# Performance work log

Hardware: AMD Instinct MI355X
Metric: run time of the kernel (lower is better)

## Reference

```python
import jax, jax.numpy as jnp
import numpy as np

N_NODES = 100000
N_EDGES = 3200000
NODE_F = 256
EDGE_F = 16
N_HEAD = 8
OUT_F = 256
NEG_SLOPE = 0.2
BN_EPS = 1e-5


def _seg_softmax(e, idx, num_segments):
    # numerically stable segment softmax over edges grouped by idx
    m = jax.ops.segment_max(e, idx, num_segments=num_segments)
    ex = jnp.exp(e - m[idx])
    s = jax.ops.segment_sum(ex, idx, num_segments=num_segments)
    return ex / s[idx]


def setup_inputs() -> dict:
    key = jax.random.key(0)
    ks = jax.random.split(key, 16)
    inp = {}
    inp["feat_src"] = jax.random.normal(ks[0], (N_NODES, NODE_F), jnp.float32)
    inp["feat_edge"] = jax.random.normal(ks[1], (N_EDGES, EDGE_F), jnp.float32)
    inp["src"] = jax.random.randint(ks[2], (N_EDGES,), 0, N_NODES, jnp.int32)
    inp["dst"] = jax.random.randint(ks[3], (N_EDGES,), 0, N_NODES, jnp.int32)
    def xav(k, fan_in, fan_out):
        # xavier_normal with relu gain sqrt(2)
        std = np.sqrt(2.0) * np.sqrt(2.0 / (fan_in + fan_out))
        return jax.random.normal(k, (fan_in, fan_out), jnp.float32) * std
    inp["W_prop_src"] = xav(ks[4], NODE_F, N_HEAD)
    inp["W_attn_src"] = xav(ks[5], NODE_F, N_HEAD)
    inp["W_attn_dst"] = xav(ks[6], NODE_F, N_HEAD)
    inp["W_attn_edge"] = xav(ks[7], EDGE_F, N_HEAD)
    inp["bn_gamma"] = jnp.ones((N_HEAD,), jnp.float32)
    inp["bn_beta"] = jnp.zeros((N_HEAD,), jnp.float32)
    inp["W_agg"] = xav(ks[8], N_HEAD, OUT_F)
    inp["b_agg"] = jnp.zeros((OUT_F,), jnp.float32)
    inp["W_apply_dst"] = xav(ks[9], NODE_F, OUT_F)
    inp["b_apply_dst"] = jnp.zeros((OUT_F,), jnp.float32)
    inp["W_apply"] = xav(ks[10], OUT_F, OUT_F)
    inp["b_apply"] = jnp.zeros((OUT_F,), jnp.float32)
    return inp


def reference(feat_src, feat_edge, src, dst, W_prop_src, W_attn_src, W_attn_dst,
              W_attn_edge, bn_gamma, bn_beta, W_agg, b_agg, W_apply_dst,
              b_apply_dst, W_apply, b_apply):
    leaky = lambda x: jnp.where(x >= 0, x, NEG_SLOPE * x)
    feat_dst = feat_src  # non-block graph
    feat_src_fc = feat_src @ W_prop_src            # [N, H]
    attn_src = feat_src @ W_attn_src               # [N, H]
    attn_dst = feat_dst @ W_attn_dst               # [N, H]
    attn_edge = feat_edge @ W_attn_edge            # [E, H]
    e = attn_src[src] + attn_dst[dst] + attn_edge  # [E, H]
    e = leaky(e)                                   # edge_att_actv = leaky_relu
    # dual softmax: geometric mean of dst- and src-normalized softmaxes
    a_dst = jnp.clip(_seg_softmax(e, dst, N_NODES), 1e-9)
    a_src = jnp.clip(_seg_softmax(e, src, N_NODES), 1e-9)
    a = jnp.sqrt(a_dst * a_src)                    # [E, H]
    msg_sum = jax.ops.segment_sum(feat_src_fc[src] * a, dst, num_segments=N_NODES)  # [N, H]
    # BatchNorm1d (training mode: batch statistics over nodes, biased var)
    mu = jnp.mean(msg_sum, axis=0)
    var = jnp.mean((msg_sum - mu) ** 2, axis=0)
    h = (msg_sum - mu) / jnp.sqrt(var + BN_EPS) * bn_gamma + bn_beta
    rst = h @ W_agg + b_agg                        # [N, OUT]
    rst = rst + feat_dst @ W_apply_dst + b_apply_dst
    rst = leaky(rst)
    rst = rst @ W_apply + b_apply
    return rst
```

## Files before the change

### kernel.cpp

```cpp
#include <hip/hip_runtime.h>

#define LRELU(x) ((x) >= 0.0f ? (x) : 0.2f * (x))

typedef __attribute__((ext_vector_type(8))) short short8;
typedef __attribute__((ext_vector_type(4))) float f32x4;

__device__ __forceinline__ unsigned short f2bf(float f) {
    union { float f; unsigned int u; } v; v.f = f;
    unsigned int u = v.u;
    u += 0x7FFFu + ((u >> 16) & 1u);
    return (unsigned short)(u >> 16);
}

__device__ __forceinline__ float bf2f(unsigned short u) {
    union { unsigned int u; float f; } v; v.u = ((unsigned int)u) << 16;
    return v.f;
}

__global__ __launch_bounds__(256) void k_nodeprep(
    const float* __restrict__ feat,
    const float* __restrict__ Wp, const float* __restrict__ Was,
    const float* __restrict__ Wad,
    float* __restrict__ fc, float* __restrict__ as_t, float* __restrict__ ad_t,
    int N, int gridN8,
    const float* __restrict__ W1, const float* __restrict__ Wagg,
    const float* __restrict__ W2,
    const float* __restrict__ b_agg, const float* __restrict__ b1,
    const float* __restrict__ b2,
    unsigned short* __restrict__ B1t, unsigned short* __restrict__ B2t,
    float* __restrict__ bias1, float* __restrict__ bias2)
{
    if ((int)blockIdx.x >= gridN8) {
        int idx = (blockIdx.x - gridN8) * 256 + threadIdx.x;
        if (idx < 73728) {
            int c = idx >> 13, rem = idx & 8191;
            int n = rem >> 5, k = rem & 31;
            float v;
            if (c < 8) v = W1[(c * 32 + k) * 256 + n];
            else       v = (k < 8) ? Wagg[k * 256 + n] : 0.f;
            B1t[idx] = f2bf(v);
        } else if (idx < 139264) {
            int j = idx - 73728;
            int c = j >> 13, rem = j & 8191;
            int n = rem >> 5, k = rem & 31;
            B2t[j] = f2bf(W2[(c * 32 + k) * 256 + n]);
        } else if (idx < 139520) {
            int n = idx - 139264;
            bias1[n] = b_agg[n] + b1[n];
        } else if (idx < 139776) {
            int n = idx - 139520;
            bias2[n] = b2[n];
        }
        return;
    }
    __shared__ float Wl[3 * 2048];
    for (int i = threadIdx.x; i < 3 * 2048; i += 256) {
        float v;
        if (i < 2048)      v = Wp[i];
        else if (i < 4096) v = Was[i - 2048];
        else               v = Wad[i - 4096];
        Wl[i] = v;
    }
    __syncthreads();
    int gid = blockIdx.x * 256 + threadIdx.x;
    int n = gid >> 3, h = gid & 7;
    if (n >= N) return;
    const float4* f4 = (const float4*)(feat + (size_t)n * 256);
    float aP = 0.f, aS = 0.f, aD = 0.f;
#pragma unroll 8
    for (int k4 = 0; k4 < 64; ++k4) {
        float4 f = f4[k4];
        int b = k4 * 32 + h;
        aP += f.x * Wl[b]        + f.y * Wl[b + 8]        + f.z * Wl[b + 16]        + f.w * Wl[b + 24];
        aS += f.x * Wl[2048 + b] + f.y * Wl[2048 + b + 8] + f.z * Wl[2048 + b + 16] + f.w * Wl[2048 + b + 24];
        aD += f.x * Wl[4096 + b] + f.y * Wl[4096 + b + 8] + f.z * Wl[4096 + b + 16] + f.w * Wl[4096 + b + 24];
    }
    fc[gid] = aP; as_t[gid] = aS; ad_t[gid] = aD;
}

__device__ __forceinline__ float edge_ex(
    const float* __restrict__ feat_edge, const float* Wl,
    const float* __restrict__ as_t, const float* __restrict__ ad_t,
    int e, int h, int s, int d)
{
    const float4* fe = (const float4*)(feat_edge + (size_t)e * 16);
    float4 f0 = fe[0], f1 = fe[1], f2 = fe[2], f3 = fe[3];
    float ae = f0.x * Wl[h]      + f0.y * Wl[h + 8]   + f0.z * Wl[h + 16]  + f0.w * Wl[h + 24]
             + f1.x * Wl[h + 32] + f1.y * Wl[h + 40]  + f1.z * Wl[h + 48]  + f1.w * Wl[h + 56]
             + f2.x * Wl[h + 64] + f2.y * Wl[h + 72]  + f2.z * Wl[h + 80]  + f2.w * Wl[h + 88]
             + f3.x * Wl[h + 96] + f3.y * Wl[h + 104] + f3.z * Wl[h + 112] + f3.w * Wl[h + 120];
    float ev = as_t[(size_t)s * 8 + h] + ad_t[(size_t)d * 8 + h] + ae;
    ev = LRELU(ev);
    return __expf(ev);
}

__global__ __launch_bounds__(256) void k_edge1(
    const float* __restrict__ feat_edge,
    const int* __restrict__ src, const int* __restrict__ dst,
    const float* __restrict__ We,
    const float* __restrict__ as_t, const float* __restrict__ ad_t,
    float* __restrict__ sum_dst, float* __restrict__ sum_src,
    unsigned short* __restrict__ exd, int E)
{
    __shared__ float Wl[128];
    if (threadIdx.x < 128) Wl[threadIdx.x] = We[threadIdx.x];
    __syncthreads();
    int gid = blockIdx.x * 256 + threadIdx.x;
    int e = gid >> 3, h = gid & 7;
    if (e >= E) return;
    int s = src[e], d = dst[e];
    float ex = edge_ex(feat_edge, Wl, as_t, ad_t, e, h, s, d);
    exd[gid] = f2bf(ex);
    atomicAdd(&sum_dst[(size_t)d * 8 + h], ex);
    atomicAdd(&sum_src[(size_t)s * 8 + h], ex);
}

__global__ __launch_bounds__(256) void k_edge2(
    const unsigned short* __restrict__ exd,
    const int* __restrict__ src, const int* __restrict__ dst,
    const float* __restrict__ sum_dst, const float* __restrict__ sum_src,
    const float* __restrict__ fc, float* __restrict__ msg, int E)
{
    int gid = blockIdx.x * 256 + threadIdx.x;
    int e = gid >> 3, h = gid & 7;
    if (e >= E) return;
    int s = src[e], d = dst[e];
    float ex = bf2f(exd[gid]);
    float Sd = sum_dst[(size_t)d * 8 + h];
    float Ss = sum_src[(size_t)s * 8 + h];
    float a_d = fmaxf(ex / Sd, 1e-9f);
    float a_s = fmaxf(ex / Ss, 1e-9f);
    atomicAdd(&msg[(size_t)d * 8 + h], fc[(size_t)s * 8 + h] * sqrtf(a_d * a_s));
}

__global__ __launch_bounds__(256) void k_bn_stats(
    const float* __restrict__ msg, float* __restrict__ accum, int N)
{
    __shared__ float s1[8], s2[8];
    if (threadIdx.x < 8) { s1[threadIdx.x] = 0.f; s2[threadIdx.x] = 0.f; }
    __syncthreads();
    int h = threadIdx.x & 7;
    float a1 = 0.f, a2 = 0.f;
    int total = N * 8;
    for (int i = blockIdx.x * 256 + threadIdx.x; i < total; i += gridDim.x * 256) {
        float x = msg[i];
        a1 += x; a2 += x * x;
    }
    atomicAdd(&s1[h], a1);
    atomicAdd(&s2[h], a2);
    __syncthreads();
    if (threadIdx.x < 8) {
        atomicAdd(&accum[threadIdx.x], s1[threadIdx.x]);
        atomicAdd(&accum[8 + threadIdx.x], s2[threadIdx.x]);
    }
}

#define ASTRIDE 296

__global__ __launch_bounds__(256, 2) void k_fused_apply(
    const float* __restrict__ feat, const float* __restrict__ msg,
    const float* __restrict__ accum,
    const float* __restrict__ gamma, const float* __restrict__ beta,
    const unsigned short* __restrict__ B1t,
    const unsigned short* __restrict__ B2t,
    const float* __restrict__ bias1, const float* __restrict__ bias2,
    float* __restrict__ out, int N)
{
    __shared__ __align__(16) unsigned short As[64 * ASTRIDE];
    __shared__ __align__(16) unsigned short Bs[8192];

    int tid = threadIdx.x;
    int row0 = blockIdx.x * 64;

#pragma unroll
    for (int t = 0; t < 16; ++t) {
        int i = tid + t * 256;
        int r = i >> 6, k4 = i & 63;
        float4 f = make_float4(0.f, 0.f, 0.f, 0.f);
        if (row0 + r < N)
            f = ((const float4*)(feat + (size_t)(row0 + r) * 256))[k4];
        ushort4 b;
        b.x = f2bf(f.x); b.y = f2bf(f.y); b.z = f2bf(f.z); b.w = f2bf(f.w);
        *(ushort4*)&As[r * ASTRIDE + k4 * 4] = b;
    }
#pragma unroll
    for (int t = 0; t < 8; ++t) {
        int e = tid + t * 256;
        int r = e >> 5, c = e & 31;
        float v = 0.f;
        if (c < 8 && row0 + r < N) {
            float invN = 1.0f / (float)N;
            float mu = accum[c] * invN;
            float var = accum[8 + c] * invN - mu * mu;
            float rstd = rsqrtf(var + 1e-5f);
            v = (msg[(size_t)(row0 + r) * 8 + c] - mu) * rstd * gamma[c] + beta[c];
        }
        As[r * ASTRIDE + 256 + c] = f2bf(v);
    }

    int wave = tid >> 6;
    int lane = tid & 63;
    int n16  = lane & 15;
    int quad = lane >> 4;
    int col0 = wave * 64;

    f32x4 acc[4][4];
#pragma unroll
    for (int rt = 0; rt < 4; ++rt)
#pragma unroll
        for (int ct = 0; ct < 4; ++ct)
            acc[rt][ct] = (f32x4){0.f, 0.f, 0.f, 0.f};

    for (int kc = 0; kc < 9; ++kc) {
        __syncthreads();
#pragma unroll
        for (int t = 0; t < 4; ++t) {
            int i = tid + t * 256;
            ((float4*)Bs)[i] = ((const float4*)(B1t + kc * 8192))[i];
        }
        __syncthreads();
        int kbase = kc * 32;
        short8 af[4], bf[4];
#pragma unroll
        for (int rt = 0; rt < 4; ++rt)
            af[rt] = *(const short8*)&As[(rt * 16 + n16) * ASTRIDE + kbase + quad * 8];
#pragma unroll
        for (int ct = 0; ct < 4; ++ct)
            bf[ct] = *(const short8*)&Bs[(col0 + ct * 16 + n16) * 32 + quad * 8];
#pragma unroll
        for (int rt = 0; rt < 4; ++rt)
#pragma unroll
            for (int ct = 0; ct < 4; ++ct)
                acc[rt][ct] = __builtin_amdgcn_mfma_f32_16x16x32_bf16(
                    af[rt], bf[ct], acc[rt][ct], 0, 0, 0);
    }

    float bi[4];
#pragma unroll
    for (int ct = 0; ct < 4; ++ct) bi[ct] = bias1[col0 + ct * 16 + n16];
    __syncthreads();
#pragma unroll
    for (int rt = 0; rt < 4; ++rt)
#pragma unroll
        for (int ct = 0; ct < 4; ++ct)
#pragma unroll
            for (int r = 0; r < 4; ++r) {
                float v = acc[rt][ct][r] + bi[ct];
                v = LRELU(v);
                int row = rt * 16 + quad * 4 + r;
                int col = col0 + ct * 16 + n16;
                As[row * ASTRIDE + col] = f2bf(v);
            }

#pragma unroll
    for (int rt = 0; rt < 4; ++rt)
#pragma unroll
        for (int ct = 0; ct < 4; ++ct)
            acc[rt][ct] = (f32x4){0.f, 0.f, 0.f, 0.f};

    for (int kc = 0; kc < 8; ++kc) {
        __syncthreads();
#pragma unroll
        for (int t = 0; t < 4; ++t) {
            int i = tid + t * 256;
            ((float4*)Bs)[i] = ((const float4*)(B2t + kc * 8192))[i];
        }
        __syncthreads();
        int kbase = kc * 32;
        short8 af[4], bf[4];
#pragma unroll
        for (int rt = 0; rt < 4; ++rt)
            af[rt] = *(const short8*)&As[(rt * 16 + n16) * ASTRIDE + kbase + quad * 8];
#pragma unroll
        for (int ct = 0; ct < 4; ++ct)
            bf[ct] = *(const short8*)&Bs[(col0 + ct * 16 + n16) * 32 + quad * 8];
#pragma unroll
        for (int rt = 0; rt < 4; ++rt)
#pragma unroll
            for (int ct = 0; ct < 4; ++ct)
                acc[rt][ct] = __builtin_amdgcn_mfma_f32_16x16x32_bf16(
                    af[rt], bf[ct], acc[rt][ct], 0, 0, 0);
    }

    float bi2[4];
#pragma unroll
    for (int ct = 0; ct < 4; ++ct) bi2[ct] = bias2[col0 + ct * 16 + n16];
#pragma unroll
    for (int rt = 0; rt < 4; ++rt)
#pragma unroll
        for (int r = 0; r < 4; ++r) {
            int row = row0 + rt * 16 + quad * 4 + r;
            if (row < N) {
#pragma unroll
                for (int ct = 0; ct < 4; ++ct) {
                    int col = col0 + ct * 16 + n16;
                    out[(size_t)row * 256 + col] = acc[rt][ct][r] + bi2[ct];
                }
            }
        }
}

extern "C" void kernel_launch(void* const* d_in, const int* in_sizes, int n_in,
                              void* d_out, int out_size, void* d_ws, size_t ws_size,
                              hipStream_t stream)
{
    const float* feat      = (const float*)d_in[0];
    const float* feat_edge = (const float*)d_in[1];
    const int*   src       = (const int*)d_in[2];
    const int*   dst       = (const int*)d_in[3];
    const float* W_prop    = (const float*)d_in[4];
    const float* W_as      = (const float*)d_in[5];
    const float* W_ad      = (const float*)d_in[6];
    const float* W_edge    = (const float*)d_in[7];
    const float* bn_gamma  = (const float*)d_in[8];
    const float* bn_beta   = (const float*)d_in[9];
    const float* W_agg     = (const float*)d_in[10];
    const float* b_agg     = (const float*)d_in[11];
    const float* W1        = (const float*)d_in[12];
    const float* b1        = (const float*)d_in[13];
    const float* W2        = (const float*)d_in[14];
    const float* b2        = (const float*)d_in[15];
    float* out = (float*)d_out;

    int N = in_sizes[0] / 256;
    int E = in_sizes[2];
    int N8 = N * 8;

    char* base = (char*)d_ws;
    size_t o = 0;
    auto take = [&](size_t bytes) -> char* {
        char* p = base + o;
        o = (o + bytes + 63) & ~(size_t)63;
        return p;
    };
    float* sum_dst = (float*)take((size_t)N8 * sizeof(float));
    float* sum_src = (float*)take((size_t)N8 * sizeof(float));
    float* msg     = (float*)take((size_t)N8 * sizeof(float));
    float* accum   = (float*)take(16 * sizeof(float));
    size_t zero_bytes = o;
    float* fc    = (float*)take((size_t)N8 * sizeof(float));
    float* as_t  = (float*)take((size_t)N8 * sizeof(float));
    float* ad_t  = (float*)take((size_t)N8 * sizeof(float));
    float* bias1 = (float*)take(256 * sizeof(float));
    float* bias2 = (float*)take(256 * sizeof(float));
    unsigned short* B1t = (unsigned short*)take(73728 * sizeof(unsigned short));
    unsigned short* B2t = (unsigned short*)take(65536 * sizeof(unsigned short));
    unsigned short* exd = (unsigned short*)take((size_t)E * 8 * sizeof(unsigned short));
    (void)ws_size;

    hipMemsetAsync(d_ws, 0, zero_bytes, stream);

    int gridN8 = (N8 + 255) / 256;
    int gridE8 = (E * 8 + 255) / 256;
    int gridF  = (N + 63) / 64;

    k_nodeprep<<<gridN8 + 546, 256, 0, stream>>>(
        feat, W_prop, W_as, W_ad, fc, as_t, ad_t, N, gridN8,
        W1, W_agg, W2, b_agg, b1, b2, B1t, B2t, bias1, bias2);
    k_edge1<<<gridE8, 256, 0, stream>>>(feat_edge, src, dst, W_edge,
                                        as_t, ad_t, sum_dst, sum_src, exd, E);
    k_edge2<<<gridE8, 256, 0, stream>>>(exd, src, dst, sum_dst, sum_src,
                                        fc, msg, E);
    k_bn_stats<<<512, 256, 0, stream>>>(msg, accum, N);
    k_fused_apply<<<gridF, 256, 0, stream>>>(feat, msg, accum, bn_gamma, bn_beta,
                                             B1t, B2t, bias1, bias2, out, N);
}
```

Before: 970.3 us.

## Factor dual-softmax normalization out of edge loop into per-node scalings

Rewrites sqrt(ex/Sd * ex/Ss) as ex * rsqrt(Ss) * rsqrt(Sd), so the per-src factor is folded into a precomputed node table g = fc*rsqrt(sum_src) and the per-dst factor is applied once per node in the BN stats pass. The edge kernel then does one gather instead of three (no sum_dst, sum_src or fc gathers per edge) and no divides or sqrt. This drops the 1e-9 clamp on each edge's attention, which changes results only when attention values are tiny. It also adds a small node-level kernel.

```diff
diff --git a/kernel.cpp b/kernel.cpp
--- a/kernel.cpp
+++ b/kernel.cpp
@@ -115,26 +115,31 @@
     atomicAdd(&sum_src[(size_t)s * 8 + h], ex);
 }
 
+__global__ __launch_bounds__(256) void k_gtab(
+    const float* __restrict__ fc, const float* __restrict__ sum_src,
+    float* __restrict__ g, int total)
+{
+    int i = blockIdx.x * 256 + threadIdx.x;
+    if (i >= total) return;
+    g[i] = fc[i] * rsqrtf(fmaxf(sum_src[i], 1e-30f));
+}
+
 __global__ __launch_bounds__(256) void k_edge2(
     const unsigned short* __restrict__ exd,
     const int* __restrict__ src, const int* __restrict__ dst,
-    const float* __restrict__ sum_dst, const float* __restrict__ sum_src,
-    const float* __restrict__ fc, float* __restrict__ msg, int E)
+    const float* __restrict__ g, float* __restrict__ U, int E)
 {
     int gid = blockIdx.x * 256 + threadIdx.x;
     int e = gid >> 3, h = gid & 7;
     if (e >= E) return;
     int s = src[e], d = dst[e];
     float ex = bf2f(exd[gid]);
-    float Sd = sum_dst[(size_t)d * 8 + h];
-    float Ss = sum_src[(size_t)s * 8 + h];
-    float a_d = fmaxf(ex / Sd, 1e-9f);
-    float a_s = fmaxf(ex / Ss, 1e-9f);
-    atomicAdd(&msg[(size_t)d * 8 + h], fc[(size_t)s * 8 + h] * sqrtf(a_d * a_s));
-}
-
-__global__ __launch_bounds__(256) void k_bn_stats(
-    const float* __restrict__ msg, float* __restrict__ accum, int N)
+    atomicAdd(&U[(size_t)d * 8 + h], ex * g[(size_t)s * 8 + h]);
+}
+
+__global__ __launch_bounds__(256) void k_bn_msg(
+    float* __restrict__ msg, const float* __restrict__ sum_dst,
+    float* __restrict__ accum, int N)
 {
     __shared__ float s1[8], s2[8];
     if (threadIdx.x < 8) { s1[threadIdx.x] = 0.f; s2[threadIdx.x] = 0.f; }
@@ -143,8 +148,9 @@
     float a1 = 0.f, a2 = 0.f;
     int total = N * 8;
     for (int i = blockIdx.x * 256 + threadIdx.x; i < total; i += gridDim.x * 256) {
-        float x = msg[i];
-        a1 += x; a2 += x * x;
+        float m = msg[i] * rsqrtf(fmaxf(sum_dst[i], 1e-30f));
+        msg[i] = m;
+        a1 += m; a2 += m * m;
     }
     atomicAdd(&s1[h], a1);
     atomicAdd(&s2[h], a2);
@@ -341,6 +347,7 @@
     float* fc    = (float*)take((size_t)N8 * sizeof(float));
     float* as_t  = (float*)take((size_t)N8 * sizeof(float));
     float* ad_t  = (float*)take((size_t)N8 * sizeof(float));
+    float* g     = (float*)take((size_t)N8 * sizeof(float));
     float* bias1 = (float*)take(256 * sizeof(float));
     float* bias2 = (float*)take(256 * sizeof(float));
     unsigned short* B1t = (unsigned short*)take(73728 * sizeof(unsigned short));
@@ -359,9 +366,9 @@
         W1, W_agg, W2, b_agg, b1, b2, B1t, B2t, bias1, bias2);
     k_edge1<<<gridE8, 256, 0, stream>>>(feat_edge, src, dst, W_edge,
                                         as_t, ad_t, sum_dst, sum_src, exd, E);
-    k_edge2<<<gridE8, 256, 0, stream>>>(exd, src, dst, sum_dst, sum_src,
-                                        fc, msg, E);
-    k_bn_stats<<<512, 256, 0, stream>>>(msg, accum, N);
+    k_gtab<<<gridN8, 256, 0, stream>>>(fc, sum_src, g, N8);
+    k_edge2<<<gridE8, 256, 0, stream>>>(exd, src, dst, g, msg, E);
+    k_bn_msg<<<512, 256, 0, stream>>>(msg, sum_dst, accum, N);
     k_fused_apply<<<gridF, 256, 0, stream>>>(feat, msg, accum, bn_gamma, bn_beta,
                                              B1t, B2t, bias1, bias2, out, N);
 }
```

Result: no change. 969.4 us (-0.1%).
